# Optimization experiments

Measured on AMD Instinct MI355X. Metric: run time of the kernel, lower is better.

The kernel has to match this reference:

```python
import jax, jax.numpy as jnp
import numpy as np

N_SEQ, N_RES, C_M = 512, 256, 256
C_OUTER, C_Z = 32, 128
LN_EPS = 1e-5
NORM_EPS = 1e-3


def setup_inputs() -> dict:
    key = jax.random.key(0)
    ks = jax.random.split(key, 6)
    f32 = jnp.float32
    return {
        "act": jax.random.normal(ks[0], (N_SEQ, N_RES, C_M), f32),
        "mask": jnp.ones((N_SEQ, N_RES), f32),
        # LayerNorm params (create_scale=True, create_offset=True)
        "ln_scale": jnp.ones((C_M,), f32),
        "ln_offset": jnp.zeros((C_M,), f32),
        # left/right projections, 'linear' (VarianceScaling fan_in scale=1)
        "left_w": (jax.random.normal(ks[1], (C_M, C_OUTER), f32) / np.float32(np.sqrt(C_M))),
        "left_b": jnp.zeros((C_OUTER,), f32),
        "right_w": (jax.random.normal(ks[2], (C_M, C_OUTER), f32) / np.float32(np.sqrt(C_M))),
        "right_b": jnp.zeros((C_OUTER,), f32),
        # output_w: VarianceScaling(scale=2.0, fan_in) over (c_outer, c_outer) input dims
        "output_w": (jax.random.normal(ks[3], (C_OUTER, C_OUTER, C_Z), f32)
                     * np.float32(np.sqrt(2.0 / (C_OUTER * C_OUTER)))),
        "output_b": jnp.zeros((C_Z,), f32),
    }


def reference(act, mask, ln_scale, ln_offset, left_w, left_b, right_w, right_b,
              output_w, output_b):
    # LayerNorm over last axis
    mu = jnp.mean(act, axis=-1, keepdims=True)
    var = jnp.var(act, axis=-1, keepdims=True)
    x = (act - mu) * jax.lax.rsqrt(var + LN_EPS) * ln_scale + ln_offset

    m = mask[..., None]  # [N_seq, N_res, 1]
    left = m * (jnp.einsum('abm,mc->abc', x, left_w) + left_b)    # [A,B,Co]
    right = m * (jnp.einsum('abm,me->abe', x, right_w) + right_b)  # [A,D,Co]

    # mean outer product: sum over MSA depth a -> [B, D, Co, Co]
    op = jnp.einsum('abc,ade->bdce', left, right)
    out = jnp.einsum('bdce,cef->bdf', op, output_w) + output_b  # [B, D, Cz]

    # normalization by pairwise mask counts
    norm = jnp.einsum('ab,ad->bd', mask, mask)[..., None]  # [B, D, 1]
    return out / (NORM_EPS + norm)
```

## Files before the change

### kernel.cpp

```cpp
#include <hip/hip_runtime.h>
#include <hip/hip_bf16.h>
#include <stdint.h>

typedef short bf16x8 __attribute__((ext_vector_type(8)));
typedef float f32x4 __attribute__((ext_vector_type(4)));
typedef unsigned short u16x4 __attribute__((ext_vector_type(4)));
typedef unsigned short u16x8 __attribute__((ext_vector_type(8)));

#define GLOAD16(g, l) __builtin_amdgcn_global_load_lds( \
    (const __attribute__((address_space(1))) void*)(g), \
    (__attribute__((address_space(3))) void*)(l), 16, 0, 0)

__device__ __forceinline__ unsigned short f2bf(float f) {
  unsigned u = __float_as_uint(f);
  unsigned r = (u + 0x7fffu + ((u >> 16) & 1u)) >> 16;
  return (unsigned short)r;
}

__global__ __launch_bounds__(256) void prep_k(
    const float* __restrict__ lw, const float* __restrict__ rw,
    const float* __restrict__ ow, unsigned short* __restrict__ Wt,
    unsigned short* __restrict__ wcombT) {
  int idx = blockIdx.x * 256 + threadIdx.x;
  if (idx < 131072) {
    int f = idx >> 10, k2 = idx & 1023;
    int e = k2 >> 5, c = k2 & 31;
    Wt[idx] = f2bf(ow[(size_t)((c << 5) + e) * 128 + f]);
  }
  if (idx < 16384) {
    int c = idx >> 8, m = idx & 255;
    wcombT[idx] = f2bf(c < 32 ? lw[m * 32 + c] : rw[m * 32 + (c - 32)]);
  }
}

__global__ __launch_bounds__(256) void norm_k(const float* __restrict__ mask,
                                              float* __restrict__ nrm) {
  int b = blockIdx.x, d = threadIdx.x;
  float s = 0.f;
  for (int a = 0; a < 512; ++a)
    s += mask[a * 256 + b] * mask[a * 256 + d];
  nrm[(b << 8) + d] = s;
}

__global__ __launch_bounds__(256) void ln_proj(
    const float* __restrict__ act, const float* __restrict__ mask,
    const float* __restrict__ lns, const float* __restrict__ lno,
    const float* __restrict__ lb, const float* __restrict__ rb,
    const unsigned short* __restrict__ wcombT,
    unsigned short* __restrict__ Lt, unsigned short* __restrict__ Rt) {
  __shared__ char smem[65536];
  const int tid = threadIdx.x;
  const int lane = tid & 63;
  const int w = tid >> 6;
  const int b = blockIdx.y;
  const int a0 = blockIdx.x << 6;
  const int r = tid >> 2;
  const int q = tid & 3;

  f32x4 xv[16];
  const float* src = act + ((size_t)(a0 + r) * 256 + b) * 256 + (q << 6);
  #pragma unroll
  for (int i = 0; i < 16; ++i) xv[i] = *(const f32x4*)(src + (i << 2));
  float s = 0.f, sq = 0.f;
  #pragma unroll
  for (int i = 0; i < 16; ++i) {
    f32x4 v = xv[i];
    s += v[0] + v[1] + v[2] + v[3];
    sq += v[0] * v[0] + v[1] * v[1] + v[2] * v[2] + v[3] * v[3];
  }
  s += __shfl_xor(s, 1); sq += __shfl_xor(sq, 1);
  s += __shfl_xor(s, 2); sq += __shfl_xor(sq, 2);
  const float mu = s * (1.f / 256.f);
  const float rs = rsqrtf(sq * (1.f / 256.f) - mu * mu + 1e-5f);

  {
    const unsigned short* wsrc = wcombT + r * 256 + (q << 6);
    #pragma unroll
    for (int i = 0; i < 8; ++i) {
      u16x8 v = *(const u16x8*)(wsrc + (i << 3));
      const int c = (q << 3) + i;
      *(u16x8*)(smem + 32768 + (r << 9) + ((c ^ (r & 7)) << 4)) = v;
    }
  }
  #pragma unroll
  for (int i = 0; i < 8; ++i) {
    u16x8 pk;
    #pragma unroll
    for (int h = 0; h < 2; ++h) {
      const int b4 = (i << 1) + h;
      const f32x4 sc = *(const f32x4*)(lns + (q << 6) + (b4 << 2));
      const f32x4 of = *(const f32x4*)(lno + (q << 6) + (b4 << 2));
      const f32x4 v = xv[b4];
      #pragma unroll
      for (int jj = 0; jj < 4; ++jj)
        pk[(h << 2) + jj] = f2bf((v[jj] - mu) * rs * sc[jj] + of[jj]);
    }
    const int c = (q << 3) + i;
    *(u16x8*)(smem + (r << 9) + ((c ^ (r & 7)) << 4)) = pk;
  }
  __syncthreads();

  const int wr = w >> 1, wc = w & 1;
  const int mrow = lane & 15, g = lane >> 4;
  f32x4 acc[2][2];
  #pragma unroll
  for (int i = 0; i < 2; ++i)
    #pragma unroll
    for (int jj = 0; jj < 2; ++jj) acc[i][jj] = (f32x4){0.f, 0.f, 0.f, 0.f};
  #pragma unroll
  for (int kk = 0; kk < 8; ++kk) {
    bf16x8 af[2], bfr[2];
    #pragma unroll
    for (int mi = 0; mi < 2; ++mi) {
      const int row = (wr << 5) + (mi << 4) + mrow;
      af[mi] = *(const bf16x8*)(smem + (row << 9) + ((((kk << 2) + g) ^ (row & 7)) << 4));
    }
    #pragma unroll
    for (int ni = 0; ni < 2; ++ni) {
      const int row = (wc << 5) + (ni << 4) + mrow;
      bfr[ni] = *(const bf16x8*)(smem + 32768 + (row << 9) + ((((kk << 2) + g) ^ (row & 7)) << 4));
    }
    #pragma unroll
    for (int mi = 0; mi < 2; ++mi)
      #pragma unroll
      for (int ni = 0; ni < 2; ++ni)
        acc[mi][ni] = __builtin_amdgcn_mfma_f32_16x16x32_bf16(af[mi], bfr[ni], acc[mi][ni], 0, 0, 0);
  }

  #pragma unroll
  for (int ni = 0; ni < 2; ++ni) {
    const int c31 = (ni << 4) + mrow;
    const float bias = (wc == 0) ? lb[c31] : rb[c31];
    unsigned short* dst = (wc == 0) ? Lt : Rt;
    #pragma unroll
    for (int mi = 0; mi < 2; ++mi) {
      u16x4 pk;
      #pragma unroll
      for (int qq = 0; qq < 4; ++qq) {
        const int ar = (wr << 5) + (mi << 4) + (g << 2) + qq;
        const float mk = mask[(size_t)(a0 + ar) * 256 + b];
        pk[qq] = f2bf((acc[mi][ni][qq] + bias) * mk);
      }
      *(u16x4*)(dst + (size_t)(b * 32 + c31) * 512 + a0 + (wr << 5) + (mi << 4) + (g << 2)) = pk;
    }
  }
}

__global__ __launch_bounds__(512, 2) void gemm_fused(
    const unsigned short* __restrict__ Lt, const unsigned short* __restrict__ Rt,
    const unsigned short* __restrict__ Wt, const float* __restrict__ nrm,
    const float* __restrict__ outb, float* __restrict__ out) {
  __shared__ char smem[131072];
  const int tid = threadIdx.x;
  const int lane = tid & 63;
  const int w = tid >> 6;
  const int wr = w >> 2, wc = w & 3;
  const int mrow = lane & 15, g = lane >> 4;

  const int bid = blockIdx.x;
  const int xcd = bid & 7, j = bid >> 3;
  const int mb = ((j >> 5) << 3) | (j & 7);
  const int nb = (xcd << 2) | ((j >> 3) & 3);
  const int m0i = mb << 8, n0i = nb << 8;

  const int srow = lane >> 3;
  const int scol = ((lane & 7) ^ srow) << 3;

  f32x4 acc[8][4];
  #pragma unroll
  for (int i = 0; i < 8; ++i)
    #pragma unroll
    for (int jj = 0; jj < 4; ++jj) acc[i][jj] = (f32x4){0.f, 0.f, 0.f, 0.f};

  {
    auto STG0 = [&](const unsigned short* gsrc, int growbase, int dstoff) {
      GLOAD16(gsrc + ((size_t)(growbase + (w << 3) + srow) << 9) + scol,
              smem + dstoff + (w << 10) + (lane << 4));
    };
    STG0(Rt, n0i, 32768);       STG0(Rt, n0i + 64, 40960);
    STG0(Rt, n0i + 128, 49152); STG0(Rt, n0i + 192, 57344);
    STG0(Lt, m0i, 0);           STG0(Lt, m0i + 128, 16384);
    STG0(Lt, m0i + 64, 8192);   STG0(Lt, m0i + 192, 24576);
  }
  asm volatile("s_waitcnt vmcnt(2)" ::: "memory");
  __builtin_amdgcn_s_barrier();

  #pragma unroll 1
  for (int t = 0; t < 8; ++t) {
    const char* bufp = smem + ((t & 1) << 16);
    const int nbuf = ((t + 1) & 1) << 16;
    const int k1 = (t + 1) << 6;
    const bool pf = (t < 7);
    auto STG = [&](const unsigned short* gsrc, int growbase, int dstoff) {
      GLOAD16(gsrc + ((size_t)(growbase + (w << 3) + srow) << 9) + k1 + scol,
              smem + nbuf + dstoff + (w << 10) + (lane << 4));
    };
    bf16x8 bfr[4][2];
    #pragma unroll
    for (int p = 0; p < 4; ++p) {
      bf16x8 af[2][2];
      #pragma unroll
      for (int mi_ = 0; mi_ < 2; ++mi_)
        #pragma unroll
        for (int kk = 0; kk < 2; ++kk) {
          const int row = (wr << 7) + (((p << 1) + mi_) << 4) + mrow;
          af[mi_][kk] = *(const bf16x8*)(bufp + (row << 7) + ((((kk << 2) + g) ^ (row & 7)) << 4));
        }
      if (p == 0) {
        #pragma unroll
        for (int ni = 0; ni < 4; ++ni)
          #pragma unroll
          for (int kk = 0; kk < 2; ++kk) {
            const int row = (wc << 6) + (ni << 4) + mrow;
            bfr[ni][kk] = *(const bf16x8*)(bufp + 32768 + (row << 7) + ((((kk << 2) + g) ^ (row & 7)) << 4));
          }
      }
      if (pf) {
        if (p == 0)      { STG(Rt, n0i, 32768);       STG(Rt, n0i + 64, 40960); }
        else if (p == 1) { STG(Rt, n0i + 128, 49152); STG(Rt, n0i + 192, 57344); }
        else if (p == 2) { STG(Lt, m0i, 0);           STG(Lt, m0i + 128, 16384); }
        else             { STG(Lt, m0i + 64, 8192);   STG(Lt, m0i + 192, 24576); }
      }
      __builtin_amdgcn_s_barrier();
      asm volatile("s_waitcnt lgkmcnt(0)" ::: "memory");
      __builtin_amdgcn_sched_barrier(0);
      __builtin_amdgcn_s_setprio(1);
      #pragma unroll
      for (int kk = 0; kk < 2; ++kk)
        #pragma unroll
        for (int mi_ = 0; mi_ < 2; ++mi_)
          #pragma unroll
          for (int ni = 0; ni < 4; ++ni)
            acc[(p << 1) + mi_][ni] = __builtin_amdgcn_mfma_f32_16x16x32_bf16(
                af[mi_][kk], bfr[ni][kk], acc[(p << 1) + mi_][ni], 0, 0, 0);
      __builtin_amdgcn_s_setprio(0);
      if (p == 1) {
        if (pf) asm volatile("s_waitcnt vmcnt(4)" ::: "memory");
        else    asm volatile("s_waitcnt vmcnt(0)" ::: "memory");
      } else if (p == 3 && pf) {
        asm volatile("s_waitcnt vmcnt(2)" ::: "memory");
      }
      __builtin_amdgcn_s_barrier();
    }
  }

  #pragma unroll
  for (int mi = 0; mi < 8; ++mi) {
    #pragma unroll
    for (int ni = 0; ni < 4; ++ni) {
      const int p = (((wr << 2) + (mi >> 1)) << 3) | ((wc << 1) + (ni >> 1));
      const int ow_ = ((ni & 1) << 10) + (mrow << 6) + ((mi & 1) << 5) + (g << 3);
      u16x4 pk;
      #pragma unroll
      for (int qq = 0; qq < 4; ++qq) pk[qq] = f2bf(acc[mi][ni][qq]);
      *(u16x4*)(smem + (p << 11) + (ow_ ^ ((p & 7) << 4) ^ (((ow_ >> 7) & 7) << 4))) = pk;
    }
  }
  __syncthreads();

  const int f0 = w << 4;
  f32x4 acc2[4];
  #pragma unroll
  for (int i = 0; i < 4; ++i) acc2[i] = (f32x4){0.f, 0.f, 0.f, 0.f};
  const unsigned short* wrow = Wt + (size_t)(f0 + mrow) * 1024;
  #pragma unroll 4
  for (int kk2 = 0; kk2 < 32; ++kk2) {
    const bf16x8 b2 = *(const bf16x8*)(wrow + (kk2 << 5) + (g << 3));
    const int orr = (kk2 << 6) + (g << 4);
    #pragma unroll
    for (int pg = 0; pg < 4; ++pg) {
      const int prow = (pg << 4) + mrow;
      const bf16x8 a2 = *(const bf16x8*)(smem + (prow << 11) +
          (orr ^ ((prow & 7) << 4) ^ (((orr >> 7) & 7) << 4)));
      acc2[pg] = __builtin_amdgcn_mfma_f32_16x16x32_bf16(a2, b2, acc2[pg], 0, 0, 0);
    }
  }

  const float ob_ = outb[f0 + mrow];
  #pragma unroll
  for (int pg = 0; pg < 4; ++pg) {
    #pragma unroll
    for (int qq = 0; qq < 4; ++qq) {
      const int p = (pg << 4) + (g << 2) + qq;
      const int f = f0 + mrow;
      const int bb = (mb << 3) + (p >> 3);
      const int dd = (nb << 3) + (p & 7);
      const float v = acc2[pg][qq] + ob_;
      out[(size_t)((bb << 8) + dd) * 128 + f] = v / (1e-3f + nrm[(bb << 8) + dd]);
    }
  }
}

extern "C" void kernel_launch(void* const* d_in, const int* in_sizes, int n_in,
                              void* d_out, int out_size, void* d_ws, size_t ws_size,
                              hipStream_t stream) {
  const float* act = (const float*)d_in[0];
  const float* mask = (const float*)d_in[1];
  const float* lns = (const float*)d_in[2];
  const float* lno = (const float*)d_in[3];
  const float* lw = (const float*)d_in[4];
  const float* lb = (const float*)d_in[5];
  const float* rw = (const float*)d_in[6];
  const float* rbv = (const float*)d_in[7];
  const float* ow = (const float*)d_in[8];
  const float* ob = (const float*)d_in[9];
  float* out = (float*)d_out;
  char* ws = (char*)d_ws;

  unsigned short* Lt = (unsigned short*)(ws);
  unsigned short* Rt = (unsigned short*)(ws + 8388608);
  unsigned short* Wt = (unsigned short*)(ws + 16777216);
  unsigned short* wcombT = (unsigned short*)(ws + 17039360);
  float* nrm = (float*)(ws + 17072128);

  hipLaunchKernelGGL(prep_k, dim3(512), dim3(256), 0, stream, lw, rw, ow, Wt, wcombT);
  hipLaunchKernelGGL(norm_k, dim3(256), dim3(256), 0, stream, mask, nrm);
  hipLaunchKernelGGL(ln_proj, dim3(8, 256), dim3(256), 0, stream,
                     act, mask, lns, lno, lb, rbv, wcombT, Lt, Rt);
  hipLaunchKernelGGL(gemm_fused, dim3(1024), dim3(512), 0, stream,
                     Lt, Rt, Wt, nrm, ob, out);
}
```

Before: 188.3 us.

## Prestage projection weights in MFMA fragment order and deepen GEMM prefetch pipeline

The prep kernel now writes the combined left/right projection weights already laid out in MFMA B-fragment order. ln_proj loads them straight from global memory, which drops the LDS staging and halves its shared memory. The main outer-product GEMM switches to per-stage 8KB LDS sub-tiles and issues loads two k-steps ahead, partly into the current buffer as soon as each part has been consumed, with retuned vmcnt waits. The aim is to hide global load latency and raise ln_proj occupancy, at the cost of intricate wait-count bookkeeping that could race or stall if miscounted.

```diff
diff --git a/kernel.cpp b/kernel.cpp
--- a/kernel.cpp
+++ b/kernel.cpp
@@ -20,7 +20,7 @@
 __global__ __launch_bounds__(256) void prep_k(
     const float* __restrict__ lw, const float* __restrict__ rw,
     const float* __restrict__ ow, unsigned short* __restrict__ Wt,
-    unsigned short* __restrict__ wcombT) {
+    unsigned short* __restrict__ wfragG) {
   int idx = blockIdx.x * 256 + threadIdx.x;
   if (idx < 131072) {
     int f = idx >> 10, k2 = idx & 1023;
@@ -28,8 +28,12 @@
     Wt[idx] = f2bf(ow[(size_t)((c << 5) + e) * 128 + f]);
   }
   if (idx < 16384) {
-    int c = idx >> 8, m = idx & 255;
-    wcombT[idx] = f2bf(c < 32 ? lw[m * 32 + c] : rw[m * 32 + (c - 32)]);
+    int frag = idx >> 9, lane = (idx >> 3) & 63, j = idx & 7;
+    int wc = frag >> 4, ni = (frag >> 3) & 1, kk = frag & 7;
+    int mrow = lane & 15, g = lane >> 4;
+    int c = wc * 32 + ni * 16 + mrow;
+    int k = kk * 32 + g * 8 + j;
+    wfragG[idx] = f2bf(c < 32 ? lw[k * 32 + c] : rw[k * 32 + (c - 32)]);
   }
 }
 
@@ -37,6 +41,7 @@
                                               float* __restrict__ nrm) {
   int b = blockIdx.x, d = threadIdx.x;
   float s = 0.f;
+  #pragma unroll 8
   for (int a = 0; a < 512; ++a)
     s += mask[a * 256 + b] * mask[a * 256 + d];
   nrm[(b << 8) + d] = s;
@@ -46,9 +51,9 @@
     const float* __restrict__ act, const float* __restrict__ mask,
     const float* __restrict__ lns, const float* __restrict__ lno,
     const float* __restrict__ lb, const float* __restrict__ rb,
-    const unsigned short* __restrict__ wcombT,
+    const unsigned short* __restrict__ wfragG,
     unsigned short* __restrict__ Lt, unsigned short* __restrict__ Rt) {
-  __shared__ char smem[65536];
+  __shared__ char smem[32768];
   const int tid = threadIdx.x;
   const int lane = tid & 63;
   const int w = tid >> 6;
@@ -73,15 +78,6 @@
   const float mu = s * (1.f / 256.f);
   const float rs = rsqrtf(sq * (1.f / 256.f) - mu * mu + 1e-5f);
 
-  {
-    const unsigned short* wsrc = wcombT + r * 256 + (q << 6);
-    #pragma unroll
-    for (int i = 0; i < 8; ++i) {
-      u16x8 v = *(const u16x8*)(wsrc + (i << 3));
-      const int c = (q << 3) + i;
-      *(u16x8*)(smem + 32768 + (r << 9) + ((c ^ (r & 7)) << 4)) = v;
-    }
-  }
   #pragma unroll
   for (int i = 0; i < 8; ++i) {
     u16x8 pk;
@@ -116,10 +112,8 @@
       af[mi] = *(const bf16x8*)(smem + (row << 9) + ((((kk << 2) + g) ^ (row & 7)) << 4));
     }
     #pragma unroll
-    for (int ni = 0; ni < 2; ++ni) {
-      const int row = (wc << 5) + (ni << 4) + mrow;
-      bfr[ni] = *(const bf16x8*)(smem + 32768 + (row << 9) + ((((kk << 2) + g) ^ (row & 7)) << 4));
-    }
+    for (int ni = 0; ni < 2; ++ni)
+      bfr[ni] = *(const bf16x8*)(wfragG + (size_t)((((wc << 1) + ni) << 3) + kk) * 512 + (lane << 3));
     #pragma unroll
     for (int mi = 0; mi < 2; ++mi)
       #pragma unroll
@@ -158,13 +152,14 @@
   const int mrow = lane & 15, g = lane >> 4;
 
   const int bid = blockIdx.x;
-  const int xcd = bid & 7, j = bid >> 3;
-  const int mb = ((j >> 5) << 3) | (j & 7);
-  const int nb = (xcd << 2) | ((j >> 3) & 3);
+  const int xcd = bid & 7, jj_ = bid >> 3;
+  const int mb = ((jj_ >> 5) << 3) | (jj_ & 7);
+  const int nb = (xcd << 2) | ((jj_ >> 3) & 3);
   const int m0i = mb << 8, n0i = nb << 8;
 
-  const int srow = lane >> 3;
-  const int scol = ((lane & 7) ^ srow) << 3;
+  const int r_l = tid >> 3;
+  const int scol = ((tid & 7) ^ (r_l & 7)) << 3;
+  const int arow_g = m0i + r_l + ((r_l & 32) ? 96 : 0);
 
   f32x4 acc[8][4];
   #pragma unroll
@@ -172,29 +167,29 @@
     #pragma unroll
     for (int jj = 0; jj < 4; ++jj) acc[i][jj] = (f32x4){0.f, 0.f, 0.f, 0.f};
 
-  {
-    auto STG0 = [&](const unsigned short* gsrc, int growbase, int dstoff) {
-      GLOAD16(gsrc + ((size_t)(growbase + (w << 3) + srow) << 9) + scol,
-              smem + dstoff + (w << 10) + (lane << 4));
-    };
-    STG0(Rt, n0i, 32768);       STG0(Rt, n0i + 64, 40960);
-    STG0(Rt, n0i + 128, 49152); STG0(Rt, n0i + 192, 57344);
-    STG0(Lt, m0i, 0);           STG0(Lt, m0i + 128, 16384);
-    STG0(Lt, m0i + 64, 8192);   STG0(Lt, m0i + 192, 24576);
-  }
-  asm volatile("s_waitcnt vmcnt(2)" ::: "memory");
+  auto STGA = [&](int buf, int p, int kt) {
+    GLOAD16(Lt + ((size_t)(arow_g + (p << 5)) << 9) + (kt << 6) + scol,
+            smem + buf + (p << 13) + (tid << 4));
+  };
+  auto STGB = [&](int buf, int q, int kt) {
+    GLOAD16(Rt + ((size_t)(n0i + (q << 6) + r_l) << 9) + (kt << 6) + scol,
+            smem + buf + 32768 + (q << 13) + (tid << 4));
+  };
+
+  #pragma unroll
+  for (int p = 0; p < 4; ++p) STGA(0, p, 0);
+  #pragma unroll
+  for (int qd = 0; qd < 4; ++qd) STGB(0, qd, 0);
+  #pragma unroll
+  for (int qd = 0; qd < 4; ++qd) STGB(65536, qd, 1);
+  STGA(65536, 0, 1); STGA(65536, 1, 1); STGA(65536, 2, 1);
+  asm volatile("s_waitcnt vmcnt(7)" ::: "memory");
   __builtin_amdgcn_s_barrier();
 
   #pragma unroll 1
   for (int t = 0; t < 8; ++t) {
-    const char* bufp = smem + ((t & 1) << 16);
+    const int cbuf = (t & 1) << 16;
     const int nbuf = ((t + 1) & 1) << 16;
-    const int k1 = (t + 1) << 6;
-    const bool pf = (t < 7);
-    auto STG = [&](const unsigned short* gsrc, int growbase, int dstoff) {
-      GLOAD16(gsrc + ((size_t)(growbase + (w << 3) + srow) << 9) + k1 + scol,
-              smem + nbuf + dstoff + (w << 10) + (lane << 4));
-    };
     bf16x8 bfr[4][2];
     #pragma unroll
     for (int p = 0; p < 4; ++p) {
@@ -203,24 +198,25 @@
       for (int mi_ = 0; mi_ < 2; ++mi_)
         #pragma unroll
         for (int kk = 0; kk < 2; ++kk) {
-          const int row = (wr << 7) + (((p << 1) + mi_) << 4) + mrow;
-          af[mi_][kk] = *(const bf16x8*)(bufp + (row << 7) + ((((kk << 2) + g) ^ (row & 7)) << 4));
+          const int loc = (wr << 5) + (mi_ << 4) + mrow;
+          af[mi_][kk] = *(const bf16x8*)(smem + cbuf + (p << 13) + (loc << 7) +
+                                         ((((kk << 2) + g) ^ (mrow & 7)) << 4));
         }
       if (p == 0) {
         #pragma unroll
         for (int ni = 0; ni < 4; ++ni)
           #pragma unroll
           for (int kk = 0; kk < 2; ++kk) {
-            const int row = (wc << 6) + (ni << 4) + mrow;
-            bfr[ni][kk] = *(const bf16x8*)(bufp + 32768 + (row << 7) + ((((kk << 2) + g) ^ (row & 7)) << 4));
+            const int loc = (ni << 4) + mrow;
+            bfr[ni][kk] = *(const bf16x8*)(smem + cbuf + 32768 + (wc << 13) + (loc << 7) +
+                                           ((((kk << 2) + g) ^ (mrow & 7)) << 4));
           }
       }
-      if (pf) {
-        if (p == 0)      { STG(Rt, n0i, 32768);       STG(Rt, n0i + 64, 40960); }
-        else if (p == 1) { STG(Rt, n0i + 128, 49152); STG(Rt, n0i + 192, 57344); }
-        else if (p == 2) { STG(Lt, m0i, 0);           STG(Lt, m0i + 128, 16384); }
-        else             { STG(Lt, m0i + 64, 8192);   STG(Lt, m0i + 192, 24576); }
-      }
+      if (p == 0) { if (t < 7) STGA(nbuf, 3, t + 1); }
+      else if (p == 1) { if (t < 6) { STGB(cbuf, 0, t + 2); STGB(cbuf, 1, t + 2); STGB(cbuf, 2, t + 2); } }
+      else if (p == 2) { if (t < 6) { STGB(cbuf, 3, t + 2); STGA(cbuf, 0, t + 2); } }
+      else { if (t < 6) { STGA(cbuf, 1, t + 2); STGA(cbuf, 2, t + 2); } }
+
       __builtin_amdgcn_s_barrier();
       asm volatile("s_waitcnt lgkmcnt(0)" ::: "memory");
       __builtin_amdgcn_sched_barrier(0);
@@ -234,11 +230,13 @@
             acc[(p << 1) + mi_][ni] = __builtin_amdgcn_mfma_f32_16x16x32_bf16(
                 af[mi_][kk], bfr[ni][kk], acc[(p << 1) + mi_][ni], 0, 0, 0);
       __builtin_amdgcn_s_setprio(0);
-      if (p == 1) {
-        if (pf) asm volatile("s_waitcnt vmcnt(4)" ::: "memory");
-        else    asm volatile("s_waitcnt vmcnt(0)" ::: "memory");
-      } else if (p == 3 && pf) {
-        asm volatile("s_waitcnt vmcnt(2)" ::: "memory");
+      if (p == 2) {
+        if (t < 6)      asm volatile("s_waitcnt vmcnt(13)" ::: "memory");
+        else if (t == 6) asm volatile("s_waitcnt vmcnt(8)" ::: "memory");
+        else            asm volatile("s_waitcnt vmcnt(0)" ::: "memory");
+      } else if (p == 3) {
+        if (t < 6)      asm volatile("s_waitcnt vmcnt(8)" ::: "memory");
+        else if (t == 6) asm volatile("s_waitcnt vmcnt(1)" ::: "memory");
       }
       __builtin_amdgcn_s_barrier();
     }
@@ -310,13 +308,13 @@
   unsigned short* Lt = (unsigned short*)(ws);
   unsigned short* Rt = (unsigned short*)(ws + 8388608);
   unsigned short* Wt = (unsigned short*)(ws + 16777216);
-  unsigned short* wcombT = (unsigned short*)(ws + 17039360);
+  unsigned short* wfragG = (unsigned short*)(ws + 17039360);
   float* nrm = (float*)(ws + 17072128);
 
-  hipLaunchKernelGGL(prep_k, dim3(512), dim3(256), 0, stream, lw, rw, ow, Wt, wcombT);
+  hipLaunchKernelGGL(prep_k, dim3(512), dim3(256), 0, stream, lw, rw, ow, Wt, wfragG);
   hipLaunchKernelGGL(norm_k, dim3(256), dim3(256), 0, stream, mask, nrm);
   hipLaunchKernelGGL(ln_proj, dim3(8, 256), dim3(256), 0, stream,
-                     act, mask, lns, lno, lb, rbv, wcombT, Lt, Rt);
+                     act, mask, lns, lno, lb, rbv, wfragG, Lt, Rt);
   hipLaunchKernelGGL(gemm_fused, dim3(1024), dim3(512), 0, stream,
                      Lt, Rt, Wt, nrm, ob, out);
 }
```

After: 185.6 us. No clear change (-1.4%).
